# Kernel optimization log

Hardware: AMD Instinct MI355X
Metric: run time of the kernel (lower is better)

## Reference

```python
import jax, jax.numpy as jnp
import numpy as np

N = 50000          # num_nodes
IN_F = 256
OUT_F = 256
R = 2
LEV = 2
L = R * LEV        # number of sparse framelet operators
NNZ = 800000       # nonzeros per operator (avg degree 16)
THRESHOLD = 1e-4


def _spmm(rows, cols, vals, x, n):
    # y = D @ x for COO sparse D of shape [n, n]
    return jax.ops.segment_sum(vals[:, None] * x[cols], rows, num_segments=n)


def setup_inputs() -> dict:
    key = jax.random.key(0)
    ks = jax.random.split(key, 7)
    x = jax.random.normal(ks[0], (N, IN_F), dtype=jnp.float32)
    # xavier-uniform-ish weight
    bound = np.sqrt(6.0 / (IN_F + OUT_F))
    weight = jax.random.uniform(ks[1], (IN_F, OUT_F), dtype=jnp.float32,
                                minval=-bound, maxval=bound)
    # filter init uniform(0.9, 1.1) as in reset_parameters
    filt = jax.random.uniform(ks[2], (R * LEV * N, 1), dtype=jnp.float32,
                              minval=0.9, maxval=1.1)
    bias = jax.random.normal(ks[3], (OUT_F,), dtype=jnp.float32) * 0.02
    # COO sparse framelet operators, scaled small to keep the chained
    # products numerically tame
    d_vals = jax.random.normal(ks[4], (L, NNZ), dtype=jnp.float32) * 0.05
    d_rows = jax.random.randint(ks[5], (L, NNZ), 0, N, dtype=jnp.int32)
    d_cols = jax.random.randint(ks[6], (L, NNZ), 0, N, dtype=jnp.int32)
    return {"x": x, "weight": weight, "filt": filt, "bias": bias,
            "d_vals": d_vals, "d_rows": d_rows, "d_cols": d_cols}


def reference(x, weight, filt, bias, d_vals, d_rows, d_cols):
    h = x @ weight                                   # [N, OUT_F]
    # fast tight-frame decomposition: chained SpMMs
    for i in range(L):
        h = _spmm(d_rows[i], d_cols[i], d_vals[i], h, N)
    # soft shrinkage
    h = jnp.sign(h) * jax.nn.relu(jnp.abs(h) - THRESHOLD)
    # learned per-row filter (first N rows of the [r*Lev*N, 1] filter)
    h = h * filt[: h.shape[0]]
    # reconstruction: operators Lev-1 .. L-1
    for i in range(LEV - 1, L):
        h = _spmm(d_rows[i], d_cols[i], d_vals[i], h, N)
    return h + bias
```

## Files before the change

### kernel.cpp

```cpp
#include <hip/hip_runtime.h>
#include <hip/hip_bf16.h>

#define N_NODES 50000
#define NNZ 800000
#define F 256
#define L_OPS 4
#define ELL_C 64
#define RTILES 3125
#define NBK 98
#define CHUNK 4096
#define CHUNKS 196

typedef unsigned int uint;
typedef unsigned short u16;
typedef unsigned char u8;
typedef unsigned long long u64;
typedef __attribute__((ext_vector_type(8))) short bf16x8;
typedef __attribute__((ext_vector_type(4))) float f32x4;
typedef __attribute__((ext_vector_type(2))) float f32x2;

#if defined(__has_builtin)
#if __has_builtin(__builtin_amdgcn_cvt_pk_f32_fp8) && \
    __has_builtin(__builtin_amdgcn_cvt_pk_fp8_f32)
#define HAS_FP8_CVT 1
#endif
#endif

__device__ inline u16 f2bf(float f) {
  return __bfloat16_as_ushort(__float2bfloat16(f));
}
__device__ inline float shrinkf(float f) {
  float t = fabsf(f) - 1e-4f;
  t = t > 0.f ? t : 0.f;
  return copysignf(t, f);
}

__device__ inline uint fp8_enc1(float f) {
#ifdef HAS_FP8_CVT
  return (uint)__builtin_amdgcn_cvt_pk_fp8_f32(f, 0.f, 0, false) & 0xFFu;
#else
  float y = f * 0x1.0p-120f;
  uint b = __float_as_uint(y);
  uint s = (b >> 24) & 0x80u;
  b &= 0x7FFFFFFFu;
  uint r = b + 0x7FFFFu + ((b >> 20) & 1u);
  return s | ((r >> 20) & 0x7Fu);
#endif
}
__device__ inline uint fp8_enc4(float a, float b, float c, float d) {
#ifdef HAS_FP8_CVT
  uint w = (uint)__builtin_amdgcn_cvt_pk_fp8_f32(a, b, 0, false);
  w = (uint)__builtin_amdgcn_cvt_pk_fp8_f32(c, d, w, true);
  return w;
#else
  return fp8_enc1(a) | (fp8_enc1(b) << 8) | (fp8_enc1(c) << 16) |
         (fp8_enc1(d) << 24);
#endif
}
__device__ inline float fp8_dec1(uint b) {
  uint u = ((b & 0x80u) << 24) | ((b & 0x7Fu) << 20);
  return __uint_as_float(u) * 0x1.0p+120f;
}

__global__ __launch_bounds__(256) void wprep_k(const float* __restrict__ W,
                                               u16* __restrict__ Wb) {
  int T = blockIdx.x * 256 + threadIdx.x;
  if (T >= 16 * 8 * 64) return;
  int lane = T & 63;
  int ks = (T >> 6) & 7;
  int ct = T >> 9;
  int k0 = ks * 32 + (lane >> 4) * 8;
  int n = ct * 16 + (lane & 15);
  u16* o = Wb + (size_t)T * 8;
#pragma unroll
  for (int j = 0; j < 8; ++j) o[j] = f2bf(W[(size_t)(k0 + j) * F + n]);
}

__global__ __launch_bounds__(256) void gemm_mfma(const float* __restrict__ X,
                                                 const u16* __restrict__ Wb,
                                                 u8* __restrict__ H) {
  const int w = threadIdx.x >> 6, lane = threadIdx.x & 63;
  const int lr = lane & 15, kg = lane >> 4;
  const int ct0 = w * 4;

  bf16x8 b[4][8];
#pragma unroll
  for (int c = 0; c < 4; ++c)
#pragma unroll
    for (int ks = 0; ks < 8; ++ks)
      b[c][ks] = *(const bf16x8*)(Wb + ((size_t)((ct0 + c) * 8 + ks) * 64 + lane) * 8);

  for (int tile = blockIdx.x; tile < RTILES; tile += gridDim.x) {
    const int rb = tile * 16;
    const float* xp = X + (size_t)(rb + lr) * F + kg * 8;
    f32x4 acc[4];
#pragma unroll
    for (int c = 0; c < 4; ++c) acc[c] = (f32x4){0.f, 0.f, 0.f, 0.f};
#pragma unroll
    for (int ks = 0; ks < 8; ++ks) {
      float4 x0 = *(const float4*)(xp + ks * 32);
      float4 x1 = *(const float4*)(xp + ks * 32 + 4);
      bf16x8 a;
      a[0] = (short)f2bf(x0.x); a[1] = (short)f2bf(x0.y);
      a[2] = (short)f2bf(x0.z); a[3] = (short)f2bf(x0.w);
      a[4] = (short)f2bf(x1.x); a[5] = (short)f2bf(x1.y);
      a[6] = (short)f2bf(x1.z); a[7] = (short)f2bf(x1.w);
#pragma unroll
      for (int c = 0; c < 4; ++c)
        acc[c] = __builtin_amdgcn_mfma_f32_16x16x32_bf16(a, b[c][ks], acc[c], 0, 0, 0);
    }
    const int r0 = rb + kg * 4;
#pragma unroll
    for (int c = 0; c < 4; ++c)
#pragma unroll
      for (int reg = 0; reg < 4; ++reg)
        H[(size_t)(r0 + reg) * F + (ct0 + c) * 16 + lr] =
            (u8)fp8_enc1(acc[c][reg] * 16.f);
  }
}

__global__ __launch_bounds__(256) void b1_hist(const int* __restrict__ rows,
                                               int* __restrict__ hoff) {
  const int op = blockIdx.y, c = blockIdx.x;
  __shared__ int h[NBK];
  for (int t = threadIdx.x; t < NBK; t += 256) h[t] = 0;
  __syncthreads();
  const int* rop = rows + (size_t)op * NNZ;
  const int base = c * CHUNK + threadIdx.x;
#pragma unroll
  for (int it = 0; it < 16; ++it) {
    int i = base + it * 256;
    if (i < NNZ) atomicAdd(&h[rop[i] >> 9], 1);
  }
  __syncthreads();
  for (int t = threadIdx.x; t < NBK; t += 256)
    hoff[((size_t)op * CHUNKS + c) * NBK + t] = h[t];
}

__global__ __launch_bounds__(512) void b2a_scan(int* __restrict__ hoff,
                                                int* __restrict__ tot) {
  const int op = blockIdx.y, b = blockIdx.x, t = threadIdx.x;
  __shared__ int sh[512];
  int v = (t < CHUNKS) ? hoff[((size_t)op * CHUNKS + t) * NBK + b] : 0;
  sh[t] = v;
  __syncthreads();
#pragma unroll
  for (int off = 1; off < 512; off <<= 1) {
    int tmp = (t >= off) ? sh[t - off] : 0;
    __syncthreads();
    sh[t] += tmp;
    __syncthreads();
  }
  if (t < CHUNKS) hoff[((size_t)op * CHUNKS + t) * NBK + b] = sh[t] - v;
  if (t == 511) tot[op * NBK + b] = sh[511];
}

__global__ __launch_bounds__(128) void b2b_base(const int* __restrict__ tot,
                                                int* __restrict__ bs) {
  const int op = blockIdx.x, t = threadIdx.x;
  __shared__ int sh[128];
  int v = (t < NBK) ? tot[op * NBK + t] : 0;
  sh[t] = v;
  __syncthreads();
#pragma unroll
  for (int off = 1; off < 128; off <<= 1) {
    int tmp = (t >= off) ? sh[t - off] : 0;
    __syncthreads();
    sh[t] += tmp;
    __syncthreads();
  }
  if (t < NBK) bs[op * NBK + t] = sh[t] - v;
}

__global__ __launch_bounds__(256) void b3_scatter(const int* __restrict__ rows,
                                                  const int* __restrict__ cols,
                                                  const float* __restrict__ vals,
                                                  const int* __restrict__ hoff,
                                                  const int* __restrict__ bs,
                                                  u64* __restrict__ part) {
  const int op = blockIdx.y, c = blockIdx.x;
  __shared__ int hist[NBK];
  __shared__ int lstart[NBK];
  __shared__ int gbase[NBK];
  __shared__ int cur[NBK];
  __shared__ int sh[256];
  __shared__ u64 stage[CHUNK];
  const int t = threadIdx.x;
  for (int k = t; k < NBK; k += 256) hist[k] = 0;
  __syncthreads();
  const int* rop = rows + (size_t)op * NNZ;
  const int* cop = cols + (size_t)op * NNZ;
  const float* vop = vals + (size_t)op * NNZ;
  const int n0 = c * CHUNK;
  const int nthis = min(CHUNK, NNZ - n0);
#pragma unroll
  for (int it = 0; it < 16; ++it) {
    int i = n0 + it * 256 + t;
    if (i < NNZ) atomicAdd(&hist[rop[i] >> 9], 1);
  }
  __syncthreads();
  int v = (t < NBK) ? hist[t] : 0;
  sh[t] = v;
  __syncthreads();
#pragma unroll
  for (int off = 1; off < 256; off <<= 1) {
    int tmp = (t >= off) ? sh[t - off] : 0;
    __syncthreads();
    sh[t] += tmp;
    __syncthreads();
  }
  if (t < NBK) {
    int ex = sh[t] - v;
    lstart[t] = ex;
    cur[t] = ex;
    gbase[t] = op * NNZ + bs[op * NBK + t] +
               hoff[((size_t)op * CHUNKS + c) * NBK + t];
  }
  __syncthreads();
#pragma unroll
  for (int it = 0; it < 16; ++it) {
    int i = n0 + it * 256 + t;
    if (i < NNZ) {
      int r = rop[i];
      int b = r >> 9;
      int p = atomicAdd(&cur[b], 1);
      uint cv = ((uint)f2bf(vop[i]) << 16) | (uint)cop[i];
      stage[p] = ((u64)cv << 32) | (uint)(b << 9) | (uint)(r & 511);
    }
  }
  __syncthreads();
  for (int q = t; q < nthis; q += 256) {
    u64 w = stage[q];
    int b = (int)((w >> 9) & 127u);
    part[(size_t)gbase[b] + (q - lstart[b])] = w;
  }
}

__global__ __launch_bounds__(256) void b4_build(const u64* __restrict__ part,
                                                const int* __restrict__ bs,
                                                const int* __restrict__ tot,
                                                uint* __restrict__ ell,
                                                int* __restrict__ cnt) {
  const int op = blockIdx.y, b = blockIdx.x;
  __shared__ int c[512];
  for (int t = threadIdx.x; t < 512; t += 256) c[t] = 0;
  __syncthreads();
  const int s = bs[op * NBK + b], n = tot[op * NBK + b];
  const u64* seg = part + (size_t)op * NNZ + s;
  uint* ellb = ell + (size_t)op * N_NODES * ELL_C + (size_t)b * 512 * ELL_C;
  for (int i = threadIdx.x; i < n; i += 256) {
    u64 w = seg[i];
    int rl = (int)(w & 0x1FFu);
    int p = atomicAdd(&c[rl], 1);
    if (p < ELL_C) ellb[rl * ELL_C + p] = (uint)(w >> 32);
  }
  __syncthreads();
  const int nrow = min(512, N_NODES - b * 512);
  int* cb = cnt + (size_t)op * N_NODES + b * 512;
  for (int t = threadIdx.x; t < nrow; t += 256) cb[t] = c[t];
}

#ifdef HAS_FP8_CVT
#define DEC4(g, lo, hi)                                                   \
  lo = __builtin_amdgcn_cvt_pk_f32_fp8((g), false);                       \
  hi = __builtin_amdgcn_cvt_pk_f32_fp8((g), true);
#else
#define DEC4(g, lo, hi)                                                   \
  lo[0] = fp8_dec1((g) & 0xFFu); lo[1] = fp8_dec1(((g) >> 8) & 0xFFu);    \
  hi[0] = fp8_dec1(((g) >> 16) & 0xFFu); hi[1] = fp8_dec1((g) >> 24);
#endif

#define PROC(cv)                                                          \
  {                                                                       \
    uint c_ = (cv) & 0xFFFFu;                                             \
    float v_ = __uint_as_float((cv) & 0xFFFF0000u);                       \
    uint g = *(const uint*)(hinL + (size_t)c_ * F);                       \
    f32x2 glo, ghi;                                                       \
    DEC4(g, glo, ghi);                                                    \
    a0 = fmaf(v_, glo[0], a0);                                            \
    a1 = fmaf(v_, glo[1], a1);                                            \
    a2 = fmaf(v_, ghi[0], a2);                                            \
    a3 = fmaf(v_, ghi[1], a3);                                            \
  }

template <int MODE>
__global__ __launch_bounds__(256) void spmm_k(const int* __restrict__ cnt,
                                              const uint* __restrict__ ell,
                                              const u8* __restrict__ hin,
                                              void* __restrict__ out,
                                              const float* __restrict__ filt,
                                              const float* __restrict__ bias,
                                              float m1, float m2) {
  const int lane = threadIdx.x & 63;
  const int r = blockIdx.x * 4 + (threadIdx.x >> 6);
  if (r >= N_NODES) return;
  int e = cnt[r];
  e = e < ELL_C ? e : ELL_C;
  const uint* __restrict__ row = ell + (size_t)r * ELL_C;
  const u8* __restrict__ hinL = hin + lane * 4;
  float a0 = 0.f, a1 = 0.f, a2 = 0.f, a3 = 0.f;
  int j = 0;
  for (; j + 8 <= e; j += 8) {
    uint4 q0 = *(const uint4*)(row + j);
    uint4 q1 = *(const uint4*)(row + j + 4);
    PROC(q0.x); PROC(q0.y); PROC(q0.z); PROC(q0.w);
    PROC(q1.x); PROC(q1.y); PROC(q1.z); PROC(q1.w);
  }
  for (; j + 4 <= e; j += 4) {
    uint4 q = *(const uint4*)(row + j);
    PROC(q.x); PROC(q.y); PROC(q.z); PROC(q.w);
  }
  for (; j < e; ++j) {
    uint cv = row[j];
    PROC(cv);
  }
  if (MODE == 0) {
    uint w = fp8_enc4(a0 * m1, a1 * m1, a2 * m1, a3 * m1);
    *(uint*)((u8*)out + (size_t)r * F + lane * 4) = w;
  } else if (MODE == 1) {
    float fl = filt[r] * m2;
    uint w = fp8_enc4(shrinkf(a0 * m1) * fl, shrinkf(a1 * m1) * fl,
                      shrinkf(a2 * m1) * fl, shrinkf(a3 * m1) * fl);
    *(uint*)((u8*)out + (size_t)r * F + lane * 4) = w;
  } else {
    float4 b = *(const float4*)(bias + lane * 4);
    float4 o;
    o.x = fmaf(a0, m1, b.x); o.y = fmaf(a1, m1, b.y);
    o.z = fmaf(a2, m1, b.z); o.w = fmaf(a3, m1, b.w);
    *(float4*)((float*)out + (size_t)r * F + lane * 4) = o;
  }
}

extern "C" void kernel_launch(void* const* d_in, const int* in_sizes, int n_in,
                              void* d_out, int out_size, void* d_ws, size_t ws_size,
                              hipStream_t stream) {
  const float* X = (const float*)d_in[0];
  const float* W = (const float*)d_in[1];
  const float* filt = (const float*)d_in[2];
  const float* bias = (const float*)d_in[3];
  const float* dvals = (const float*)d_in[4];
  const int* drows = (const int*)d_in[5];
  const int* dcols = (const int*)d_in[6];

  char* p = (char*)d_ws;
  auto alloc = [&](size_t bytes) {
    char* q = p;
    p += (bytes + 255) & ~(size_t)255;
    return q;
  };
  u8* hA = (u8*)alloc((size_t)N_NODES * F);
  u8* hB = (u8*)alloc((size_t)N_NODES * F);
  u16* Wb = (u16*)alloc((size_t)F * F * 2);
  int* cnt = (int*)alloc((size_t)L_OPS * N_NODES * 4);
  uint* ell = (uint*)alloc((size_t)L_OPS * N_NODES * ELL_C * 4);
  u64* part = (u64*)alloc((size_t)L_OPS * NNZ * 8);
  int* hoff = (int*)alloc((size_t)L_OPS * CHUNKS * NBK * 4);
  int* tot = (int*)alloc((size_t)L_OPS * NBK * 4);
  int* bs = (int*)alloc((size_t)L_OPS * NBK * 4);

  b1_hist<<<dim3(CHUNKS, L_OPS), 256, 0, stream>>>(drows, hoff);
  b2a_scan<<<dim3(NBK, L_OPS), 512, 0, stream>>>(hoff, tot);
  b2b_base<<<L_OPS, 128, 0, stream>>>(tot, bs);
  b3_scatter<<<dim3(CHUNKS, L_OPS), 256, 0, stream>>>(drows, dcols, dvals,
                                                      hoff, bs, part);
  b4_build<<<dim3(NBK, L_OPS), 256, 0, stream>>>(part, bs, tot, ell, cnt);

  wprep_k<<<64, 256, 0, stream>>>(W, Wb);
  gemm_mfma<<<1024, 256, 0, stream>>>(X, Wb, hA);

  auto sp = [&](int op, const u8* in, void* out, int mode, float m1, float m2) {
    const int* co = cnt + (size_t)op * N_NODES;
    const uint* eo = ell + (size_t)op * N_NODES * ELL_C;
    dim3 g((N_NODES + 3) / 4);
    if (mode == 0)
      spmm_k<0><<<g, 256, 0, stream>>>(co, eo, in, out, filt, bias, m1, m2);
    else if (mode == 1)
      spmm_k<1><<<g, 256, 0, stream>>>(co, eo, in, out, filt, bias, m1, m2);
    else
      spmm_k<2><<<g, 256, 0, stream>>>(co, eo, in, out, filt, bias, m1, m2);
  };

  sp(0, hA, hB, 0, 4.f, 0.f);
  sp(1, hB, hA, 0, 4.f, 0.f);
  sp(2, hA, hB, 0, 4.f, 0.f);
  sp(3, hB, hA, 1, 0x1.0p-10f, 0x1.0p+13f);
  sp(1, hA, hB, 0, 4.f, 0.f);
  sp(2, hB, hA, 0, 4.f, 0.f);
  sp(3, hA, d_out, 2, 0x1.0p-17f, 0.f);
}
```

Measured before the change: 318.9 us.

## Stage GEMM operands in LDS, split output columns across grid, prefetch next X tile

The dense X@W GEMM now splits the 256 output columns into two halves across blockIdx.y, with each block copying its half of the bf16 weights into shared memory instead of holding them in registers. The X tile is loaded with coalesced float4 reads, converted to bf16 and staged in padded LDS, and the next tile's loads are issued before the MFMA loop so they overlap with compute. This lowers register pressure and improves global read coalescing. In exchange, each block adds two barriers per tile, and the GEMM is only a small share of a pipeline dominated by SpMM.

```diff
diff --git a/kernel.cpp b/kernel.cpp
--- a/kernel.cpp
+++ b/kernel.cpp
@@ -79,43 +79,63 @@
 __global__ __launch_bounds__(256) void gemm_mfma(const float* __restrict__ X,
                                                  const u16* __restrict__ Wb,
                                                  u8* __restrict__ H) {
-  const int w = threadIdx.x >> 6, lane = threadIdx.x & 63;
-  const int lr = lane & 15, kg = lane >> 4;
-  const int ct0 = w * 4;
-
-  bf16x8 b[4][8];
-#pragma unroll
-  for (int c = 0; c < 4; ++c)
-#pragma unroll
-    for (int ks = 0; ks < 8; ++ks)
-      b[c][ks] = *(const bf16x8*)(Wb + ((size_t)((ct0 + c) * 8 + ks) * 64 + lane) * 8);
-
-  for (int tile = blockIdx.x; tile < RTILES; tile += gridDim.x) {
-    const int rb = tile * 16;
-    const float* xp = X + (size_t)(rb + lr) * F + kg * 8;
-    f32x4 acc[4];
-#pragma unroll
-    for (int c = 0; c < 4; ++c) acc[c] = (f32x4){0.f, 0.f, 0.f, 0.f};
+  const int tid = threadIdx.x;
+  const int w = tid >> 6, lane = tid & 63;
+  const int half = blockIdx.y;
+  const int ct0 = half * 8 + w * 2;
+
+  __shared__ u16 Bs[8 * 8 * 64 * 8];
+  __shared__ u16 Xs[16 * 264];
+
+  {
+    const uint4* src = (const uint4*)(Wb + (size_t)half * (8 * 8 * 64 * 8));
+    uint4* dst = (uint4*)Bs;
+#pragma unroll
+    for (int i = 0; i < 16; ++i) dst[tid + i * 256] = src[tid + i * 256];
+  }
+
+  const int xrow = tid >> 4, xkc = (tid & 15) * 16;
+  float4 xr0, xr1, xr2, xr3;
+  int tile = blockIdx.x;
+  {
+    const float4* xp = (const float4*)(X + (size_t)(tile * 16 + xrow) * F + xkc);
+    xr0 = xp[0]; xr1 = xp[1]; xr2 = xp[2]; xr3 = xp[3];
+  }
+
+  for (; tile < RTILES; tile += gridDim.x) {
+    __syncthreads();
+    u16 tb[16];
+    tb[0] = f2bf(xr0.x); tb[1] = f2bf(xr0.y); tb[2] = f2bf(xr0.z); tb[3] = f2bf(xr0.w);
+    tb[4] = f2bf(xr1.x); tb[5] = f2bf(xr1.y); tb[6] = f2bf(xr1.z); tb[7] = f2bf(xr1.w);
+    tb[8] = f2bf(xr2.x); tb[9] = f2bf(xr2.y); tb[10] = f2bf(xr2.z); tb[11] = f2bf(xr2.w);
+    tb[12] = f2bf(xr3.x); tb[13] = f2bf(xr3.y); tb[14] = f2bf(xr3.z); tb[15] = f2bf(xr3.w);
+    *(uint4*)(Xs + xrow * 264 + xkc) = *(uint4*)tb;
+    *(uint4*)(Xs + xrow * 264 + xkc + 8) = *(uint4*)(tb + 8);
+    __syncthreads();
+
+    int nt = tile + gridDim.x;
+    if (nt < RTILES) {
+      const float4* xp = (const float4*)(X + (size_t)(nt * 16 + xrow) * F + xkc);
+      xr0 = xp[0]; xr1 = xp[1]; xr2 = xp[2]; xr3 = xp[3];
+    }
+
+    f32x4 acc0 = (f32x4){0.f, 0.f, 0.f, 0.f};
+    f32x4 acc1 = (f32x4){0.f, 0.f, 0.f, 0.f};
 #pragma unroll
     for (int ks = 0; ks < 8; ++ks) {
-      float4 x0 = *(const float4*)(xp + ks * 32);
-      float4 x1 = *(const float4*)(xp + ks * 32 + 4);
-      bf16x8 a;
-      a[0] = (short)f2bf(x0.x); a[1] = (short)f2bf(x0.y);
-      a[2] = (short)f2bf(x0.z); a[3] = (short)f2bf(x0.w);
-      a[4] = (short)f2bf(x1.x); a[5] = (short)f2bf(x1.y);
-      a[6] = (short)f2bf(x1.z); a[7] = (short)f2bf(x1.w);
-#pragma unroll
-      for (int c = 0; c < 4; ++c)
-        acc[c] = __builtin_amdgcn_mfma_f32_16x16x32_bf16(a, b[c][ks], acc[c], 0, 0, 0);
+      bf16x8 a = *(const bf16x8*)(Xs + (lane & 15) * 264 + ks * 32 + (lane >> 4) * 8);
+      bf16x8 b0 = *(const bf16x8*)(Bs + ((size_t)((w * 2 + 0) * 8 + ks) * 64 + lane) * 8);
+      bf16x8 b1 = *(const bf16x8*)(Bs + ((size_t)((w * 2 + 1) * 8 + ks) * 64 + lane) * 8);
+      acc0 = __builtin_amdgcn_mfma_f32_16x16x32_bf16(a, b0, acc0, 0, 0, 0);
+      acc1 = __builtin_amdgcn_mfma_f32_16x16x32_bf16(a, b1, acc1, 0, 0, 0);
     }
-    const int r0 = rb + kg * 4;
-#pragma unroll
-    for (int c = 0; c < 4; ++c)
-#pragma unroll
-      for (int reg = 0; reg < 4; ++reg)
-        H[(size_t)(r0 + reg) * F + (ct0 + c) * 16 + lr] =
-            (u8)fp8_enc1(acc[c][reg] * 16.f);
+    const int r0 = tile * 16 + (lane >> 4) * 4;
+    const int lr = lane & 15;
+#pragma unroll
+    for (int reg = 0; reg < 4; ++reg) {
+      H[(size_t)(r0 + reg) * F + (ct0 + 0) * 16 + lr] = (u8)fp8_enc1(acc0[reg] * 16.f);
+      H[(size_t)(r0 + reg) * F + (ct0 + 1) * 16 + lr] = (u8)fp8_enc1(acc1[reg] * 16.f);
+    }
   }
 }
 
@@ -366,7 +386,7 @@
   b4_build<<<dim3(NBK, L_OPS), 256, 0, stream>>>(part, bs, tot, ell, cnt);
 
   wprep_k<<<64, 256, 0, stream>>>(W, Wb);
-  gemm_mfma<<<1024, 256, 0, stream>>>(X, Wb, hA);
+  gemm_mfma<<<dim3(512, 2), 256, 0, stream>>>(X, Wb, hA);
 
   auto sp = [&](int op, const u8* in, void* out, int mode, float m1, float m2) {
     const int* co = cnt + (size_t)op * N_NODES;
```

Result: faster. 306.0 us (-4.1%).
